# Performance work log

Measured on AMD Instinct MI355X. Metric: run time of the kernel, lower is better.

## Reference

```python
import jax, jax.numpy as jnp
import numpy as np

B, S, D = 64, 4096, 64          # bsz*n_heads, seq_len, head_size
WINDOW = 256                    # num_toks_attended
NEG = -10000.0


def setup_inputs() -> dict:
    key = jax.random.key(0)
    kq, kk, kv = jax.random.split(key, 3)
    q = jax.random.normal(kq, (B, S, D), dtype=jnp.float32)
    k = jax.random.normal(kk, (B, S, D), dtype=jnp.float32)
    v = jax.random.normal(kv, (B, S, D), dtype=jnp.float32)
    return {"q": q, "k": k, "v": v}


def reference(q, k, v):
    # sliding_window_attn, topk_for_softmax=-1 (plain softmax)
    b, s, d = q.shape
    hw = WINDOW // 2                       # half window = 128
    n = s // hw                            # number of half-window bins
    split = lambda x: x.reshape(b, n, hw, d)
    bq, bk, bv = split(q), split(k), split(v)

    def cat_half_neighbours(x):
        # left-rolled, self, right-rolled half-bins -> [b, n, 3*hw, d]
        return jnp.concatenate(
            (jnp.roll(x, 1, axis=1), x, jnp.roll(x, -1, axis=1)), axis=-2)

    bk = cat_half_neighbours(bk)
    bv = cat_half_neighbours(bv)

    dots = jnp.einsum('bnid,bnjd->bnij', bq, bk) * (d ** -0.5)  # [b,n,hw,3hw]

    # mask: strict lower triangle on left block, none on middle,
    # upper-incl-diagonal on right block (as in the torch code)
    lmask = jnp.tril(jnp.ones((hw, hw), dtype=bool), -1)
    mask = jnp.concatenate((lmask, jnp.zeros_like(lmask), ~lmask), axis=-1)
    dots = jnp.where(mask, NEG, dots)

    p = jax.nn.softmax(dots, axis=-1)
    bo = jnp.einsum('bnij,bnjd->bnid', p, bv)
    return bo.reshape(b, s, d)
```

## Files before the change

### kernel.cpp

```cpp
#include <hip/hip_runtime.h>
#include <hip/hip_bf16.h>
#include <stdint.h>

using f32x4  = __attribute__((ext_vector_type(4))) float;
using bf16x8 = __attribute__((ext_vector_type(8))) __bf16;
using bf16x4 = __attribute__((ext_vector_type(4))) __bf16;
using bf16x2 = __attribute__((ext_vector_type(2))) __bf16;
typedef unsigned int u32;

#define SEQ 4096

__device__ __forceinline__ void mfma16(f32x4& acc, bf16x4 a, bf16x4 b) {
    asm volatile("v_mfma_f32_16x16x16_bf16 %0, %1, %2, %0"
                 : "+v"(acc) : "v"(a), "v"(b));
}

__global__ __launch_bounds__(256, 2) void lattn_kern(
        const float* __restrict__ Q, const float* __restrict__ K,
        const float* __restrict__ V, float* __restrict__ O)
{
    __shared__ __bf16 Kl[320 * 64];
    __shared__ __bf16 Vt[64 * 320];

    const int tid  = threadIdx.x;
    const int wv   = tid >> 6;
    const int lane = tid & 63;
    const int g    = lane >> 4;
    const int c    = lane & 15;
    const u32 swc  = (u32)(c & 7);

    const int b    = blockIdx.x >> 3;
    const int oct  = blockIdx.x & 7;
    const size_t baseB = (size_t)b * (SEQ * 64);
    const int t00  = oct * 512;

    int r0 = (t00 + SEQ - 128) % 320;

    #pragma unroll
    for (int it = 0; it < 10; ++it) {
        const int ch = tid + it * 256;
        const int j = ch >> 3, dg = ch & 7;
        const int grow = (t00 - 128 + j) & (SEQ - 1);
        int row = r0 + j; if (row >= 320) row -= 320;
        const float* src = K + baseB + (size_t)grow * 64 + dg * 8;
        f32x4 k0 = *(const f32x4*)src, k1 = *(const f32x4*)(src + 4);
        bf16x8 hk;
        #pragma unroll
        for (int u = 0; u < 4; ++u) { hk[u] = (__bf16)k0[u]; hk[u + 4] = (__bf16)k1[u]; }
        *(bf16x8*)((char*)Kl + row * 128 + (((u32)dg ^ (u32)(row & 7)) << 4)) = hk;
    }
    #pragma unroll
    for (int it = 0; it < 5; ++it) {
        const int ch = tid + it * 256;
        const int rp = ch >> 3, dg = ch & 7;
        const int grow = (t00 - 128 + 2 * rp) & (SEQ - 1);
        int col = r0 + 2 * rp; if (col >= 320) col -= 320;
        const float* src = V + baseB + (size_t)grow * 64 + dg * 8;
        f32x4 a0 = *(const f32x4*)src,        a1 = *(const f32x4*)(src + 4);
        f32x4 b0 = *(const f32x4*)(src + 64), b1 = *(const f32x4*)(src + 68);
        #pragma unroll
        for (int u = 0; u < 8; ++u) {
            const int d = dg * 8 + u;
            bf16x2 pv;
            pv[0] = (__bf16)((u < 4) ? a0[u] : a1[u - 4]);
            pv[1] = (__bf16)((u < 4) ? b0[u] : b1[u - 4]);
            const u32 sw = (u32)(u ^ dg);
            *(bf16x2*)((char*)Vt + (((u32)d * 640u + (u32)col * 2u) ^ (sw << 4))) = pv;
        }
    }

    bf16x8 aq0, aq1;
    {
        const float* qp = Q + baseB + (size_t)(t00 + wv * 16 + c) * 64 + g * 8;
        f32x4 q0 = *(const f32x4*)qp,        q1 = *(const f32x4*)(qp + 4);
        f32x4 q2 = *(const f32x4*)(qp + 32), q3 = *(const f32x4*)(qp + 36);
        #pragma unroll
        for (int u = 0; u < 4; ++u) {
            aq0[u] = (__bf16)q0[u]; aq0[u + 4] = (__bf16)q1[u];
            aq1[u] = (__bf16)q2[u]; aq1[u + 4] = (__bf16)q3[u];
        }
    }

    for (int i = 0; i < 8; ++i) {
        const int t0 = t00 + i * 64;
        __syncthreads();

        f32x4 s_[17];
        const int rb = r0 + 16 * wv + c;
        __builtin_amdgcn_s_setprio(1);
        #pragma unroll
        for (int lt = 0; lt < 17; ++lt) {
            int row = rb + 16 * lt; if (row >= 320) row -= 320;
            const char* ka = (const char*)Kl + (u32)row * 128u;
            bf16x8 a0 = *(const bf16x8*)(ka + (((u32)g ^ swc) << 4));
            bf16x8 a1 = *(const bf16x8*)(ka + (((u32)(g + 4) ^ swc) << 4));
            f32x4 acc = {0.f, 0.f, 0.f, 0.f};
            acc = __builtin_amdgcn_mfma_f32_16x16x32_bf16(a0, aq0, acc, 0, 0, 0);
            acc = __builtin_amdgcn_mfma_f32_16x16x32_bf16(a1, aq1, acc, 0, 0, 0);
            s_[lt] = acc;
        }
        __builtin_amdgcn_s_setprio(0);

        f32x4 qn0, qn1, qn2, qn3, dk[4], dv[4];
        int krow0 = 0, krow1 = 0, vcol = 0, kdg = 0, vdg = 0;
        if (i < 7) {
            const float* qp = Q + baseB + (size_t)(t0 + 64 + wv * 16 + c) * 64 + g * 8;
            qn0 = *(const f32x4*)qp;        qn1 = *(const f32x4*)(qp + 4);
            qn2 = *(const f32x4*)(qp + 32); qn3 = *(const f32x4*)(qp + 36);
            {
                const int jj = tid >> 3; kdg = tid & 7;
                const int grow0 = (t0 + 192 + jj) & (SEQ - 1);
                const float* s0 = K + baseB + (size_t)grow0 * 64 + kdg * 8;
                dk[0] = *(const f32x4*)s0; dk[1] = *(const f32x4*)(s0 + 4);
                krow0 = r0 + jj;
                const int grow1 = (t0 + 192 + jj + 32) & (SEQ - 1);
                const float* s1 = K + baseB + (size_t)grow1 * 64 + kdg * 8;
                dk[2] = *(const f32x4*)s1; dk[3] = *(const f32x4*)(s1 + 4);
                krow1 = r0 + jj + 32;
            }
            {
                const int rp = tid >> 3; vdg = tid & 7;
                const int grow = (t0 + 192 + 2 * rp) & (SEQ - 1);
                const float* s0 = V + baseB + (size_t)grow * 64 + vdg * 8;
                dv[0] = *(const f32x4*)s0;        dv[1] = *(const f32x4*)(s0 + 4);
                dv[2] = *(const f32x4*)(s0 + 64); dv[3] = *(const f32x4*)(s0 + 68);
                vcol = r0 + 2 * rp;
            }
        }

        const int k4 = 4 * g;
        float sum = 0.f;
        #pragma unroll
        for (int lt = 0; lt < 17; ++lt) {
            #pragma unroll
            for (int r = 0; r < 4; ++r) {
                float e = exp2f(s_[lt][r] * 0.18033688f);
                if (lt == 0)  e = (k4 + r <  c) ? 0.f : e;
                if (lt == 16) e = (k4 + r >= c) ? 0.f : e;
                s_[lt][r] = e; sum += e;
            }
        }
        sum += __shfl_xor(sum, 16, 64);
        sum += __shfl_xor(sum, 32, 64);
        const float inv = 1.0f / sum;

        bf16x4 pa[17];
        #pragma unroll
        for (int lt = 0; lt < 17; ++lt) {
            #pragma unroll
            for (int r = 0; r < 4; ++r) pa[lt][r] = (__bf16)(s_[lt][r] * inv);
        }

        f32x4 o[4] = {{0,0,0,0},{0,0,0,0},{0,0,0,0},{0,0,0,0}};
        const int cb = r0 + 16 * wv + 4 * g;
        __builtin_amdgcn_s_setprio(1);
        #pragma unroll
        for (int lt = 0; lt < 17; ++lt) {
            int col = cb + 16 * lt; if (col >= 320) col -= 320;
            #pragma unroll
            for (int dt = 0; dt < 4; ++dt) {
                const int d  = dt * 16 + c;
                const u32 sw = (u32)((d & 7) ^ ((d >> 3) & 7));
                const u32 vb = ((u32)d * 640u + (u32)col * 2u) ^ (sw << 4);
                const bf16x4 vbf = *(const bf16x4*)((const char*)Vt + vb);
                mfma16(o[dt], pa[lt], vbf);
            }
        }
        __builtin_amdgcn_s_setprio(0);
        asm volatile("s_nop 7\n\ts_nop 7" ::);

        #pragma unroll
        for (int dt = 0; dt < 4; ++dt) {
            #pragma unroll
            for (int r = 0; r < 4; ++r) {
                const int row = t0 + wv * 16 + 4 * g + r;
                O[baseB + (size_t)row * 64 + dt * 16 + c] = o[dt][r];
            }
        }

        if (i < 7) {
            __syncthreads();
            bf16x8 hk;
            #pragma unroll
            for (int u = 0; u < 4; ++u) { hk[u] = (__bf16)dk[0][u]; hk[u + 4] = (__bf16)dk[1][u]; }
            *(bf16x8*)((char*)Kl + krow0 * 128 + (((u32)kdg ^ (u32)(krow0 & 7)) << 4)) = hk;
            #pragma unroll
            for (int u = 0; u < 4; ++u) { hk[u] = (__bf16)dk[2][u]; hk[u + 4] = (__bf16)dk[3][u]; }
            *(bf16x8*)((char*)Kl + krow1 * 128 + (((u32)kdg ^ (u32)(krow1 & 7)) << 4)) = hk;
            #pragma unroll
            for (int u = 0; u < 8; ++u) {
                const int d = vdg * 8 + u;
                bf16x2 pv;
                pv[0] = (__bf16)((u < 4) ? dv[0][u] : dv[1][u - 4]);
                pv[1] = (__bf16)((u < 4) ? dv[2][u] : dv[3][u - 4]);
                const u32 sw = (u32)(u ^ vdg);
                *(bf16x2*)((char*)Vt + (((u32)d * 640u + (u32)vcol * 2u) ^ (sw << 4))) = pv;
            }
            r0 += 64; if (r0 >= 320) r0 -= 320;
            #pragma unroll
            for (int u = 0; u < 4; ++u) {
                aq0[u] = (__bf16)qn0[u]; aq0[u + 4] = (__bf16)qn1[u];
                aq1[u] = (__bf16)qn2[u]; aq1[u + 4] = (__bf16)qn3[u];
            }
        }
    }
}

extern "C" void kernel_launch(void* const* d_in, const int* in_sizes, int n_in,
                              void* d_out, int out_size, void* d_ws, size_t ws_size,
                              hipStream_t stream) {
    const float* q = (const float*)d_in[0];
    const float* k = (const float*)d_in[1];
    const float* v = (const float*)d_in[2];
    float* o = (float*)d_out;
    const int nB = in_sizes[0] / (SEQ * 64);
    dim3 grid(nB * 8), block(256);
    hipLaunchKernelGGL(lattn_kern, grid, block, 0, stream, q, k, v, o);
}
```

Measured before the change: 71.69 us.

## Replace sliding-window ring buffer loop with one-shot 1024-thread blocks per 256 queries

Drops the persistent 8-iteration loop, where each 256-thread block streamed K/V through a 320-row ring buffer. Instead, each 1024-thread block loads a full 512-row K/V halo window once and processes 256 queries in a single pass. It also remaps block indices so neighbouring query blocks land on the same XCD for L2 reuse, and replaces the XOR-swizzled V layout with a padded one. The aim is to remove per-iteration barriers and serial pipelining and expose more parallelism. The cost is roughly doubled K/V global reads from the overlapping halo, about 130 KB of LDS per block (one block per CU), and possible register pressure under the new launch bounds.

```diff
diff --git a/kernel.cpp b/kernel.cpp
--- a/kernel.cpp
+++ b/kernel.cpp
@@ -15,12 +15,12 @@
                  : "+v"(acc) : "v"(a), "v"(b));
 }
 
-__global__ __launch_bounds__(256, 2) void lattn_kern(
+__global__ __launch_bounds__(1024, 4) void lattn_kern(
         const float* __restrict__ Q, const float* __restrict__ K,
         const float* __restrict__ V, float* __restrict__ O)
 {
-    __shared__ __bf16 Kl[320 * 64];
-    __shared__ __bf16 Vt[64 * 320];
+    __shared__ __bf16 Kl[512 * 64];
+    __shared__ __bf16 Vt[64 * 520];
 
     const int tid  = threadIdx.x;
     const int wv   = tid >> 6;
@@ -29,19 +29,18 @@
     const int c    = lane & 15;
     const u32 swc  = (u32)(c & 7);
 
-    const int b    = blockIdx.x >> 3;
-    const int oct  = blockIdx.x & 7;
+    const int obid = blockIdx.x;
+    const int bid  = (obid & 7) * 128 + (obid >> 3);
+    const int b    = bid >> 4;
+    const int qb   = bid & 15;
+    const int t0   = qb * 256;
     const size_t baseB = (size_t)b * (SEQ * 64);
-    const int t00  = oct * 512;
-
-    int r0 = (t00 + SEQ - 128) % 320;
 
     #pragma unroll
-    for (int it = 0; it < 10; ++it) {
-        const int ch = tid + it * 256;
-        const int j = ch >> 3, dg = ch & 7;
-        const int grow = (t00 - 128 + j) & (SEQ - 1);
-        int row = r0 + j; if (row >= 320) row -= 320;
+    for (int it = 0; it < 4; ++it) {
+        const int ch  = tid + it * 1024;
+        const int row = ch >> 3, dg = ch & 7;
+        const int grow = (t0 - 128 + row) & (SEQ - 1);
         const float* src = K + baseB + (size_t)grow * 64 + dg * 8;
         f32x4 k0 = *(const f32x4*)src, k1 = *(const f32x4*)(src + 4);
         bf16x8 hk;
@@ -49,12 +48,12 @@
         for (int u = 0; u < 4; ++u) { hk[u] = (__bf16)k0[u]; hk[u + 4] = (__bf16)k1[u]; }
         *(bf16x8*)((char*)Kl + row * 128 + (((u32)dg ^ (u32)(row & 7)) << 4)) = hk;
     }
+
     #pragma unroll
-    for (int it = 0; it < 5; ++it) {
-        const int ch = tid + it * 256;
+    for (int it = 0; it < 2; ++it) {
+        const int ch = tid + it * 1024;
         const int rp = ch >> 3, dg = ch & 7;
-        const int grow = (t00 - 128 + 2 * rp) & (SEQ - 1);
-        int col = r0 + 2 * rp; if (col >= 320) col -= 320;
+        const int grow = (t0 - 128 + 2 * rp) & (SEQ - 1);
         const float* src = V + baseB + (size_t)grow * 64 + dg * 8;
         f32x4 a0 = *(const f32x4*)src,        a1 = *(const f32x4*)(src + 4);
         f32x4 b0 = *(const f32x4*)(src + 64), b1 = *(const f32x4*)(src + 68);
@@ -64,14 +63,13 @@
             bf16x2 pv;
             pv[0] = (__bf16)((u < 4) ? a0[u] : a1[u - 4]);
             pv[1] = (__bf16)((u < 4) ? b0[u] : b1[u - 4]);
-            const u32 sw = (u32)(u ^ dg);
-            *(bf16x2*)((char*)Vt + (((u32)d * 640u + (u32)col * 2u) ^ (sw << 4))) = pv;
+            *(bf16x2*)((char*)Vt + (u32)d * 1040u + (u32)rp * 4u) = pv;
         }
     }
 
     bf16x8 aq0, aq1;
     {
-        const float* qp = Q + baseB + (size_t)(t00 + wv * 16 + c) * 64 + g * 8;
+        const float* qp = Q + baseB + (size_t)(t0 + wv * 16 + c) * 64 + g * 8;
         f32x4 q0 = *(const f32x4*)qp,        q1 = *(const f32x4*)(qp + 4);
         f32x4 q2 = *(const f32x4*)(qp + 32), q3 = *(const f32x4*)(qp + 36);
         #pragma unroll
@@ -81,127 +79,69 @@
         }
     }
 
-    for (int i = 0; i < 8; ++i) {
-        const int t0 = t00 + i * 64;
-        __syncthreads();
+    __syncthreads();
 
-        f32x4 s_[17];
-        const int rb = r0 + 16 * wv + c;
-        __builtin_amdgcn_s_setprio(1);
+    f32x4 s_[17];
+    __builtin_amdgcn_s_setprio(1);
+    #pragma unroll
+    for (int lt = 0; lt < 17; ++lt) {
+        const int row = 16 * wv + c + 16 * lt;
+        const char* ka = (const char*)Kl + (u32)row * 128u;
+        bf16x8 a0 = *(const bf16x8*)(ka + (((u32)g ^ swc) << 4));
+        bf16x8 a1 = *(const bf16x8*)(ka + (((u32)(g + 4) ^ swc) << 4));
+        f32x4 acc = {0.f, 0.f, 0.f, 0.f};
+        acc = __builtin_amdgcn_mfma_f32_16x16x32_bf16(a0, aq0, acc, 0, 0, 0);
+        acc = __builtin_amdgcn_mfma_f32_16x16x32_bf16(a1, aq1, acc, 0, 0, 0);
+        s_[lt] = acc;
+    }
+    __builtin_amdgcn_s_setprio(0);
+
+    const int k4 = 4 * g;
+    float sum = 0.f;
+    #pragma unroll
+    for (int lt = 0; lt < 17; ++lt) {
         #pragma unroll
-        for (int lt = 0; lt < 17; ++lt) {
-            int row = rb + 16 * lt; if (row >= 320) row -= 320;
-            const char* ka = (const char*)Kl + (u32)row * 128u;
-            bf16x8 a0 = *(const bf16x8*)(ka + (((u32)g ^ swc) << 4));
-            bf16x8 a1 = *(const bf16x8*)(ka + (((u32)(g + 4) ^ swc) << 4));
-            f32x4 acc = {0.f, 0.f, 0.f, 0.f};
-            acc = __builtin_amdgcn_mfma_f32_16x16x32_bf16(a0, aq0, acc, 0, 0, 0);
-            acc = __builtin_amdgcn_mfma_f32_16x16x32_bf16(a1, aq1, acc, 0, 0, 0);
-            s_[lt] = acc;
+        for (int r = 0; r < 4; ++r) {
+            float e = exp2f(s_[lt][r] * 0.18033688f);
+            if (lt == 0)  e = (k4 + r <  c) ? 0.f : e;
+            if (lt == 16) e = (k4 + r >= c) ? 0.f : e;
+            s_[lt][r] = e; sum += e;
         }
-        __builtin_amdgcn_s_setprio(0);
+    }
+    sum += __shfl_xor(sum, 16, 64);
+    sum += __shfl_xor(sum, 32, 64);
+    const float inv = 1.0f / sum;
 
-        f32x4 qn0, qn1, qn2, qn3, dk[4], dv[4];
-        int krow0 = 0, krow1 = 0, vcol = 0, kdg = 0, vdg = 0;
-        if (i < 7) {
-            const float* qp = Q + baseB + (size_t)(t0 + 64 + wv * 16 + c) * 64 + g * 8;
-            qn0 = *(const f32x4*)qp;        qn1 = *(const f32x4*)(qp + 4);
-            qn2 = *(const f32x4*)(qp + 32); qn3 = *(const f32x4*)(qp + 36);
-            {
-                const int jj = tid >> 3; kdg = tid & 7;
-                const int grow0 = (t0 + 192 + jj) & (SEQ - 1);
-                const float* s0 = K + baseB + (size_t)grow0 * 64 + kdg * 8;
-                dk[0] = *(const f32x4*)s0; dk[1] = *(const f32x4*)(s0 + 4);
-                krow0 = r0 + jj;
-                const int grow1 = (t0 + 192 + jj + 32) & (SEQ - 1);
-                const float* s1 = K + baseB + (size_t)grow1 * 64 + kdg * 8;
-                dk[2] = *(const f32x4*)s1; dk[3] = *(const f32x4*)(s1 + 4);
-                krow1 = r0 + jj + 32;
-            }
-            {
-                const int rp = tid >> 3; vdg = tid & 7;
-                const int grow = (t0 + 192 + 2 * rp) & (SEQ - 1);
-                const float* s0 = V + baseB + (size_t)grow * 64 + vdg * 8;
-                dv[0] = *(const f32x4*)s0;        dv[1] = *(const f32x4*)(s0 + 4);
-                dv[2] = *(const f32x4*)(s0 + 64); dv[3] = *(const f32x4*)(s0 + 68);
-                vcol = r0 + 2 * rp;
-            }
-        }
+    bf16x4 pa[17];
+    #pragma unroll
+    for (int lt = 0; lt < 17; ++lt) {
+        #pragma unroll
+        for (int r = 0; r < 4; ++r) pa[lt][r] = (__bf16)(s_[lt][r] * inv);
+    }
 
-        const int k4 = 4 * g;
-        float sum = 0.f;
-        #pragma unroll
-        for (int lt = 0; lt < 17; ++lt) {
-            #pragma unroll
-            for (int r = 0; r < 4; ++r) {
-                float e = exp2f(s_[lt][r] * 0.18033688f);
-                if (lt == 0)  e = (k4 + r <  c) ? 0.f : e;
-                if (lt == 16) e = (k4 + r >= c) ? 0.f : e;
-                s_[lt][r] = e; sum += e;
-            }
-        }
-        sum += __shfl_xor(sum, 16, 64);
-        sum += __shfl_xor(sum, 32, 64);
-        const float inv = 1.0f / sum;
-
-        bf16x4 pa[17];
-        #pragma unroll
-        for (int lt = 0; lt < 17; ++lt) {
-            #pragma unroll
-            for (int r = 0; r < 4; ++r) pa[lt][r] = (__bf16)(s_[lt][r] * inv);
-        }
-
-        f32x4 o[4] = {{0,0,0,0},{0,0,0,0},{0,0,0,0},{0,0,0,0}};
-        const int cb = r0 + 16 * wv + 4 * g;
-        __builtin_amdgcn_s_setprio(1);
-        #pragma unroll
-        for (int lt = 0; lt < 17; ++lt) {
-            int col = cb + 16 * lt; if (col >= 320) col -= 320;
-            #pragma unroll
-            for (int dt = 0; dt < 4; ++dt) {
-                const int d  = dt * 16 + c;
-                const u32 sw = (u32)((d & 7) ^ ((d >> 3) & 7));
-                const u32 vb = ((u32)d * 640u + (u32)col * 2u) ^ (sw << 4);
-                const bf16x4 vbf = *(const bf16x4*)((const char*)Vt + vb);
-                mfma16(o[dt], pa[lt], vbf);
-            }
-        }
-        __builtin_amdgcn_s_setprio(0);
-        asm volatile("s_nop 7\n\ts_nop 7" ::);
-
+    f32x4 o[4] = {{0,0,0,0},{0,0,0,0},{0,0,0,0},{0,0,0,0}};
+    const int cb = 16 * wv + 4 * g;
+    __builtin_amdgcn_s_setprio(1);
+    #pragma unroll
+    for (int lt = 0; lt < 17; ++lt) {
+        const int col = cb + 16 * lt;
         #pragma unroll
         for (int dt = 0; dt < 4; ++dt) {
-            #pragma unroll
-            for (int r = 0; r < 4; ++r) {
-                const int row = t0 + wv * 16 + 4 * g + r;
-                O[baseB + (size_t)row * 64 + dt * 16 + c] = o[dt][r];
-            }
+            const int d = dt * 16 + c;
+            const bf16x4 vbf = *(const bf16x4*)((const char*)Vt
+                                + (u32)d * 1040u + (u32)col * 2u);
+            mfma16(o[dt], pa[lt], vbf);
         }
+    }
+    __builtin_amdgcn_s_setprio(0);
+    asm volatile("s_nop 7\n\ts_nop 7" ::);
 
-        if (i < 7) {
-            __syncthreads();
-            bf16x8 hk;
-            #pragma unroll
-            for (int u = 0; u < 4; ++u) { hk[u] = (__bf16)dk[0][u]; hk[u + 4] = (__bf16)dk[1][u]; }
-            *(bf16x8*)((char*)Kl + krow0 * 128 + (((u32)kdg ^ (u32)(krow0 & 7)) << 4)) = hk;
-            #pragma unroll
-            for (int u = 0; u < 4; ++u) { hk[u] = (__bf16)dk[2][u]; hk[u + 4] = (__bf16)dk[3][u]; }
-            *(bf16x8*)((char*)Kl + krow1 * 128 + (((u32)kdg ^ (u32)(krow1 & 7)) << 4)) = hk;
-            #pragma unroll
-            for (int u = 0; u < 8; ++u) {
-                const int d = vdg * 8 + u;
-                bf16x2 pv;
-                pv[0] = (__bf16)((u < 4) ? dv[0][u] : dv[1][u - 4]);
-                pv[1] = (__bf16)((u < 4) ? dv[2][u] : dv[3][u - 4]);
-                const u32 sw = (u32)(u ^ vdg);
-                *(bf16x2*)((char*)Vt + (((u32)d * 640u + (u32)vcol * 2u) ^ (sw << 4))) = pv;
-            }
-            r0 += 64; if (r0 >= 320) r0 -= 320;
-            #pragma unroll
-            for (int u = 0; u < 4; ++u) {
-                aq0[u] = (__bf16)qn0[u]; aq0[u + 4] = (__bf16)qn1[u];
-                aq1[u] = (__bf16)qn2[u]; aq1[u + 4] = (__bf16)qn3[u];
-            }
+    #pragma unroll
+    for (int dt = 0; dt < 4; ++dt) {
+        #pragma unroll
+        for (int r = 0; r < 4; ++r) {
+            const int row = t0 + wv * 16 + 4 * g + r;
+            O[baseB + (size_t)row * 64 + dt * 16 + c] = o[dt][r];
         }
     }
 }
@@ -214,6 +154,6 @@
     const float* v = (const float*)d_in[2];
     float* o = (float*)d_out;
     const int nB = in_sizes[0] / (SEQ * 64);
-    dim3 grid(nB * 8), block(256);
+    dim3 grid(nB * 16), block(1024);
     hipLaunchKernelGGL(lattn_kern, grid, block, 0, stream, q, k, v, o);
 }
```

Measured after the change: 79.18 us. 10.4% more time.
